# Optimization experiments

Measured on AMD Instinct MI355X. Metric: run time of the kernel, lower is better.

## Reference

```python
import jax, jax.numpy as jnp
import numpy as np

D_MODEL = 1024
N_HEADS = 16
HEAD_DIM = D_MODEL // N_HEADS
WINDOW = 256
N_GLOBAL = 2
EPS = 1e-5


def _layernorm(x, g, b):
    mu = jnp.mean(x, axis=-1, keepdims=True)
    var = jnp.var(x, axis=-1, keepdims=True)
    return (x - mu) * jax.lax.rsqrt(var + EPS) * g + b


def _longformer_mask(T):
    i = jnp.arange(T)[:, None]
    j = jnp.arange(T)[None, :]
    half = WINDOW // 2
    local = (j >= i - half) & (j <= i + half)
    glob = jnp.zeros((T, T), dtype=bool)
    if N_GLOBAL >= 1:
        glob = glob | (i == 0) | (j == 0)
    if N_GLOBAL >= 2 and T > 1:
        glob = glob | (i == T - 1) | (j == T - 1)
    allowed = (local | glob) & (j <= i)  # causal
    neg_inf = jnp.float32(-jnp.inf)
    return jnp.where(allowed, jnp.float32(0.0), neg_inf)[None, None]  # (1,1,T,T)


def setup_inputs() -> dict:
    key = jax.random.key(0)
    ks = jax.random.split(key, 8)
    B, T, D = 2, 2048, D_MODEL
    s = 0.02
    return {
        "x": jax.random.normal(ks[0], (B, T, D), dtype=jnp.float32),
        "ln1_g": jnp.ones((D,), jnp.float32),
        "ln1_b": jnp.zeros((D,), jnp.float32),
        "ln2_g": jnp.ones((D,), jnp.float32),
        "ln2_b": jnp.zeros((D,), jnp.float32),
        "Wq": jax.random.normal(ks[1], (D, D), jnp.float32) * s,
        "Wk": jax.random.normal(ks[2], (D, D), jnp.float32) * s,
        "Wv": jax.random.normal(ks[3], (D, D), jnp.float32) * s,
        "Wo": jax.random.normal(ks[4], (D, D), jnp.float32) * s,
        "bo": jnp.zeros((D,), jnp.float32),
        "W1": jax.random.normal(ks[5], (D, 4 * D), jnp.float32) * s,
        "b1": jnp.zeros((4 * D,), jnp.float32),
        "W2": jax.random.normal(ks[6], (4 * D, D), jnp.float32) * s,
        "b2": jnp.zeros((D,), jnp.float32),
    }


def reference(x, ln1_g, ln1_b, ln2_g, ln2_b, Wq, Wk, Wv, Wo, bo, W1, b1, W2, b2):
    B, T, D = x.shape
    h = _layernorm(x, ln1_g, ln1_b)
    # (B,T,D) -> (B,H,T,hd)
    q = (h @ Wq).reshape(B, T, N_HEADS, HEAD_DIM).transpose(0, 2, 1, 3)
    k = (h @ Wk).reshape(B, T, N_HEADS, HEAD_DIM).transpose(0, 2, 1, 3)
    v = (h @ Wv).reshape(B, T, N_HEADS, HEAD_DIM).transpose(0, 2, 1, 3)
    mask = _longformer_mask(T)
    scores = jnp.einsum("bhqd,bhkd->bhqk", q, k) / np.sqrt(HEAD_DIM) + mask
    attn = jax.nn.softmax(scores, axis=-1)
    out = jnp.einsum("bhqk,bhkd->bhqd", attn, v)
    out = out.transpose(0, 2, 1, 3).reshape(B, T, D)
    x = x + out @ Wo + bo
    h2 = _layernorm(x, ln2_g, ln2_b)
    ffn = jax.nn.gelu(h2 @ W1 + b1, approximate=False) @ W2 + b2
    return x + ffn
```

## Files before the change

kernel.cpp:

```cpp
#include <hip/hip_runtime.h>
#include <cmath>

#define Tseq 2048
#define Dm   1024
#define NHd  16
#define HDim 64
#define Mrows 4096
#define QS   3072
#define PAD  72
#define NSPLIT 16

typedef _Float16 f16;
typedef _Float16 half8 __attribute__((ext_vector_type(8)));
typedef _Float16 half4 __attribute__((ext_vector_type(4)));
typedef float    floatx4 __attribute__((ext_vector_type(4)));

#define ASYNC_COPY16(g, l)                                                       \
  __builtin_amdgcn_global_load_lds((const __attribute__((address_space(1))) void*)(g), \
                                   (__attribute__((address_space(3))) void*)(l), 16, 0, 0)

__device__ __forceinline__ float gelu_f(float v) {
  const float u = 0.7978845608028654f * (v + 0.044715f * v * v * v);
  const float e = __expf(2.0f * u);
  return 0.5f * v * (2.0f - 2.0f / (e + 1.0f));
}

__global__ __launch_bounds__(256) void transp_f16(const float* __restrict__ W,
                                                  f16* __restrict__ Wt, int K, int N) {
  __shared__ float tile[32][33];
  const int n0 = blockIdx.x * 32, k0 = blockIdx.y * 32;
  const int tx = threadIdx.x & 31, ty = threadIdx.x >> 5;
#pragma unroll
  for (int i = 0; i < 32; i += 8)
    tile[ty + i][tx] = W[(size_t)(k0 + ty + i) * N + n0 + tx];
  __syncthreads();
#pragma unroll
  for (int i = 0; i < 32; i += 8)
    Wt[(size_t)(n0 + ty + i) * K + k0 + tx] = (f16)tile[tx][ty + i];
}

__global__ __launch_bounds__(256) void transp_qkv(const float* __restrict__ Wq,
                                                  const float* __restrict__ Wk,
                                                  const float* __restrict__ Wv,
                                                  f16* __restrict__ Wt) {
  __shared__ float tile[32][33];
  const float* W = (blockIdx.z == 0) ? Wq : (blockIdx.z == 1) ? Wk : Wv;
  f16* dst = Wt + (size_t)blockIdx.z * Dm * Dm;
  const int n0 = blockIdx.x * 32, k0 = blockIdx.y * 32;
  const int tx = threadIdx.x & 31, ty = threadIdx.x >> 5;
#pragma unroll
  for (int i = 0; i < 32; i += 8)
    tile[ty + i][tx] = W[(size_t)(k0 + ty + i) * Dm + n0 + tx];
  __syncthreads();
#pragma unroll
  for (int i = 0; i < 32; i += 8)
    dst[(size_t)(n0 + ty + i) * Dm + k0 + tx] = (f16)tile[tx][ty + i];
}

__global__ __launch_bounds__(256) void ln_f16(const float* __restrict__ x,
                                              const float* __restrict__ g,
                                              const float* __restrict__ bb,
                                              f16* __restrict__ out) {
  const int row = blockIdx.x, t = threadIdx.x;
  const float4 v = ((const float4*)(x + (size_t)row * Dm))[t];
  float s  = v.x + v.y + v.z + v.w;
  float ss = v.x * v.x + v.y * v.y + v.z * v.z + v.w * v.w;
#pragma unroll
  for (int m = 32; m >= 1; m >>= 1) { s += __shfl_xor(s, m); ss += __shfl_xor(ss, m); }
  __shared__ float red[8];
  if ((t & 63) == 0) { red[t >> 6] = s; red[4 + (t >> 6)] = ss; }
  __syncthreads();
  const float S  = red[0] + red[1] + red[2] + red[3];
  const float SS = red[4] + red[5] + red[6] + red[7];
  const float mean = S * (1.0f / Dm);
  const float inv  = rsqrtf(SS * (1.0f / Dm) - mean * mean + 1e-5f);
  const float4 gg = ((const float4*)g)[t];
  const float4 bv = ((const float4*)bb)[t];
  half4 o;
  o.x = (f16)(((v.x - mean) * inv) * gg.x + bv.x);
  o.y = (f16)(((v.y - mean) * inv) * gg.y + bv.y);
  o.z = (f16)(((v.z - mean) * inv) * gg.z + bv.z);
  o.w = (f16)(((v.w - mean) * inv) * gg.w + bv.w);
  *((half4*)(out + (size_t)row * Dm) + t) = o;
}

template <int NS>
__global__ __launch_bounds__(256) void reduce_ln(const f16* __restrict__ P,
                                                 const float* __restrict__ resid,
                                                 const float* __restrict__ bias,
                                                 const float* __restrict__ g,
                                                 const float* __restrict__ bb,
                                                 float* __restrict__ x1,
                                                 f16* __restrict__ h) {
  const int row = blockIdx.x, t = threadIdx.x;
  const size_t idx = (size_t)row * (Dm / 4) + t;
  const float4 r = ((const float4*)resid)[idx];
  const float4 b = ((const float4*)bias)[t];
  float4 o; o.x = r.x + b.x; o.y = r.y + b.y; o.z = r.z + b.z; o.w = r.w + b.w;
#pragma unroll
  for (int z = 0; z < NS; ++z) {
    const half4 p = ((const half4*)(P + (size_t)z * Mrows * Dm))[idx];
    o.x += (float)p[0]; o.y += (float)p[1]; o.z += (float)p[2]; o.w += (float)p[3];
  }
  ((float4*)x1)[idx] = o;
  float s  = o.x + o.y + o.z + o.w;
  float ss = o.x * o.x + o.y * o.y + o.z * o.z + o.w * o.w;
#pragma unroll
  for (int m = 32; m >= 1; m >>= 1) { s += __shfl_xor(s, m); ss += __shfl_xor(ss, m); }
  __shared__ float red[8];
  if ((t & 63) == 0) { red[t >> 6] = s; red[4 + (t >> 6)] = ss; }
  __syncthreads();
  const float S  = red[0] + red[1] + red[2] + red[3];
  const float SS = red[4] + red[5] + red[6] + red[7];
  const float mean = S * (1.0f / Dm);
  const float inv  = rsqrtf(SS * (1.0f / Dm) - mean * mean + 1e-5f);
  const float4 gg = ((const float4*)g)[t];
  const float4 bv = ((const float4*)bb)[t];
  half4 oh;
  oh[0] = (f16)(((o.x - mean) * inv) * gg.x + bv.x);
  oh[1] = (f16)(((o.y - mean) * inv) * gg.y + bv.y);
  oh[2] = (f16)(((o.z - mean) * inv) * gg.z + bv.z);
  oh[3] = (f16)(((o.w - mean) * inv) * gg.w + bv.w);
  ((half4*)h)[idx] = oh;
}

template <int NS>
__global__ __launch_bounds__(256) void reduceK(const f16* __restrict__ P,
                                               const float* __restrict__ resid,
                                               const float* __restrict__ bias,
                                               float* __restrict__ out) {
  const int t = blockIdx.x * 256 + threadIdx.x;
  const int col4 = t & (Dm / 4 - 1);
  const float4 r = ((const float4*)resid)[t];
  const float4 b = ((const float4*)bias)[col4];
  float4 o; o.x = r.x + b.x; o.y = r.y + b.y; o.z = r.z + b.z; o.w = r.w + b.w;
#pragma unroll
  for (int z = 0; z < NS; ++z) {
    const half4 p = ((const half4*)(P + (size_t)z * Mrows * Dm))[t];
    o.x += (float)p[0]; o.y += (float)p[1]; o.z += (float)p[2]; o.w += (float)p[3];
  }
  ((float4*)out)[t] = o;
}

template <int EPI>
__global__ __launch_bounds__(256, 4) void gemm_f16(const f16* __restrict__ A,
                                                   const f16* __restrict__ Bt,
                                                   int M, int N, int K, int kLen,
                                                   const float* __restrict__ bias,
                                                   f16* __restrict__ Ch) {
  __shared__ f16 As[128 * 64];
  __shared__ f16 Bs[128 * 64];
  const int tid = threadIdx.x;
  const int m0 = blockIdx.y * 128, n0 = blockIdx.x * 128;
  const int kOff = blockIdx.z * kLen;
  const int w = tid >> 6, l = tid & 63;
  const int wr = (w >> 1) * 64, wc = (w & 1) * 64;
  const int c = l & 15, qq = l >> 4;
  const int cx = c & 7;
  const int srow = tid >> 3;
  const int scol = ((tid & 7) ^ (srow & 7)) * 8;

  floatx4 acc[4][4] = {};

  const f16* Ab = A + (size_t)(m0 + srow) * K + kOff + scol;
  const f16* Bb = Bt + (size_t)(n0 + srow) * K + kOff + scol;

  for (int k0 = 0; k0 < kLen; k0 += 64) {
    __syncthreads();
#pragma unroll
    for (int i = 0; i < 4; ++i) {
      ASYNC_COPY16(Ab + k0 + (size_t)(i * 32) * K, As + i * 2048 + w * 512);
      ASYNC_COPY16(Bb + k0 + (size_t)(i * 32) * K, Bs + i * 2048 + w * 512);
    }
    __syncthreads();
    half8 af[4][2], bfr[4][2];
#pragma unroll
    for (int t = 0; t < 4; ++t) {
      const int ra = (wr + t * 16 + c) * 64;
      af[t][0] = *(const half8*)&As[ra + ((qq ^ cx) * 8)];
      af[t][1] = *(const half8*)&As[ra + (((4 + qq) ^ cx) * 8)];
      const int rb = (wc + t * 16 + c) * 64;
      bfr[t][0] = *(const half8*)&Bs[rb + ((qq ^ cx) * 8)];
      bfr[t][1] = *(const half8*)&Bs[rb + (((4 + qq) ^ cx) * 8)];
    }
#pragma unroll
    for (int ti = 0; ti < 4; ++ti)
#pragma unroll
      for (int tj = 0; tj < 4; ++tj) {
        acc[ti][tj] = __builtin_amdgcn_mfma_f32_16x16x32_f16(af[ti][0], bfr[tj][0], acc[ti][tj], 0, 0, 0);
        acc[ti][tj] = __builtin_amdgcn_mfma_f32_16x16x32_f16(af[ti][1], bfr[tj][1], acc[ti][tj], 0, 0, 0);
      }
  }

  f16* Cw = (EPI == 5) ? (Ch + (size_t)blockIdx.z * M * N) : Ch;
#pragma unroll
  for (int ti = 0; ti < 4; ++ti)
#pragma unroll
    for (int tj = 0; tj < 4; ++tj)
#pragma unroll
      for (int r = 0; r < 4; ++r) {
        const int row = m0 + wr + ti * 16 + qq * 4 + r;
        const int col = n0 + wc + tj * 16 + c;
        const size_t idx = (size_t)row * N + col;
        float v = acc[ti][tj][r];
        if (EPI == 2) {
          Cw[idx] = (f16)gelu_f(v + bias[col]);
        } else {
          Cw[idx] = (f16)v;
        }
      }
}

__global__ __launch_bounds__(256, 4) void attn_win(const f16* __restrict__ qkv,
                                                   f16* __restrict__ ao) {
  __shared__ f16 qs[64 * PAD];
  __shared__ f16 ks[64 * PAD];
  __shared__ f16 vts[64 * PAD];
  __shared__ f16 ps[64 * PAD];
  const int qt = blockIdx.x;
  const int b = blockIdx.y >> 4, hh = blockIdx.y & 15;
  const int q0 = qt * 64;
  const int tid = threadIdx.x, w = tid >> 6, l = tid & 63;
  const int c = l & 15, qq = l >> 4;
  const int wr = w * 16;
  const size_t base = ((size_t)b * Tseq) * QS + hh * HDim;
  const int rr = tid >> 2, ss = (tid & 3) * 16;

  {
    const f16* src = qkv + base + (size_t)(q0 + rr) * QS + ss;
    *(uint4*)&qs[rr * PAD + ss]     = *(const uint4*)src;
    *(uint4*)&qs[rr * PAD + ss + 8] = *(const uint4*)(src + 8);
  }

  float m_run[4], l_run[4];
  floatx4 oacc[4];
#pragma unroll
  for (int r = 0; r < 4; ++r) { m_run[r] = -INFINITY; l_run[r] = 0.f; }
#pragma unroll
  for (int td = 0; td < 4; ++td) oacc[td] = (floatx4){0.f, 0.f, 0.f, 0.f};

  int chunks[4]; int nch = 0;
  if (qt > 2) chunks[nch++] = 0;
  for (int ch = (qt - 2 > 0 ? qt - 2 : 0); ch <= qt; ++ch) chunks[nch++] = ch;

  for (int ci = 0; ci < nch; ++ci) {
    const int j0 = chunks[ci] * 64;
    __syncthreads();
    {
      const f16* srck = qkv + base + 1024 + (size_t)(j0 + rr) * QS + ss;
      *(uint4*)&ks[rr * PAD + ss]     = *(const uint4*)srck;
      *(uint4*)&ks[rr * PAD + ss + 8] = *(const uint4*)(srck + 8);
      const f16* srcv = qkv + base + 2048 + (size_t)(j0 + rr) * QS + ss;
      uint4 va0 = *(const uint4*)srcv;
      uint4 va1 = *(const uint4*)(srcv + 8);
      const f16* e0 = (const f16*)&va0;
      const f16* e1 = (const f16*)&va1;
#pragma unroll
      for (int i = 0; i < 8; ++i) vts[(ss + i) * PAD + rr] = e0[i];
#pragma unroll
      for (int i = 0; i < 8; ++i) vts[(ss + 8 + i) * PAD + rr] = e1[i];
    }
    __syncthreads();

    const half8 a0 = *(const half8*)&qs[(wr + c) * PAD + qq * 8];
    const half8 a1 = *(const half8*)&qs[(wr + c) * PAD + 32 + qq * 8];
    floatx4 sacc[4];
#pragma unroll
    for (int tj = 0; tj < 4; ++tj) {
      const half8 b0 = *(const half8*)&ks[(tj * 16 + c) * PAD + qq * 8];
      const half8 b1 = *(const half8*)&ks[(tj * 16 + c) * PAD + 32 + qq * 8];
      floatx4 s4 = {0.f, 0.f, 0.f, 0.f};
      s4 = __builtin_amdgcn_mfma_f32_16x16x32_f16(a0, b0, s4, 0, 0, 0);
      s4 = __builtin_amdgcn_mfma_f32_16x16x32_f16(a1, b1, s4, 0, 0, 0);
      sacc[tj] = s4;
    }

#pragma unroll
    for (int r = 0; r < 4; ++r) {
      const int ii = q0 + wr + qq * 4 + r;
      float sv[4];
      float mx = -INFINITY;
#pragma unroll
      for (int tj = 0; tj < 4; ++tj) {
        const int jj = j0 + tj * 16 + c;
        const bool allowed = (jj <= ii) && ((ii - jj) <= 128 || jj == 0);
        sv[tj] = allowed ? sacc[tj][r] * 0.125f : -INFINITY;
        mx = fmaxf(mx, sv[tj]);
      }
#pragma unroll
      for (int mm = 8; mm >= 1; mm >>= 1) mx = fmaxf(mx, __shfl_xor(mx, mm));
      const float mn = fmaxf(m_run[r], mx);
      const float alpha = (mn == -INFINITY) ? 1.f : __expf(m_run[r] - mn);
      float sum = 0.f;
      float p[4];
#pragma unroll
      for (int tj = 0; tj < 4; ++tj) { p[tj] = __expf(sv[tj] - mn); sum += p[tj]; }
#pragma unroll
      for (int mm = 8; mm >= 1; mm >>= 1) sum += __shfl_xor(sum, mm);
      l_run[r] = l_run[r] * alpha + sum;
      m_run[r] = mn;
#pragma unroll
      for (int td = 0; td < 4; ++td) oacc[td][r] *= alpha;
#pragma unroll
      for (int tj = 0; tj < 4; ++tj)
        ps[(wr + qq * 4 + r) * PAD + tj * 16 + c] = (f16)p[tj];
    }

    const half8 p0 = *(const half8*)&ps[(wr + c) * PAD + qq * 8];
    const half8 p1 = *(const half8*)&ps[(wr + c) * PAD + 32 + qq * 8];
#pragma unroll
    for (int td = 0; td < 4; ++td) {
      const half8 b0 = *(const half8*)&vts[(td * 16 + c) * PAD + qq * 8];
      const half8 b1 = *(const half8*)&vts[(td * 16 + c) * PAD + 32 + qq * 8];
      oacc[td] = __builtin_amdgcn_mfma_f32_16x16x32_f16(p0, b0, oacc[td], 0, 0, 0);
      oacc[td] = __builtin_amdgcn_mfma_f32_16x16x32_f16(p1, b1, oacc[td], 0, 0, 0);
    }
  }

#pragma unroll
  for (int td = 0; td < 4; ++td)
#pragma unroll
    for (int r = 0; r < 4; ++r) {
      const int ii = q0 + wr + qq * 4 + r;
      ao[((size_t)(b * Tseq + ii)) * Dm + hh * HDim + td * 16 + c] =
          (f16)(oacc[td][r] / l_run[r]);
    }
}

__global__ __launch_bounds__(256) void attn_row_part(const f16* __restrict__ qkv,
                                                     float* __restrict__ part) {
  const int bh = blockIdx.x, sp = blockIdx.y;
  const int b = bh >> 4, hh = bh & 15;
  const int tid = threadIdx.x;
  const size_t base = ((size_t)b * Tseq) * QS + hh * HDim;
  const int j0 = sp * (Tseq / NSPLIT);
  __shared__ float qsh[64];
  __shared__ float ps[128];
  __shared__ float red[4];
  __shared__ float red2[4];
  __shared__ float oacc[4][64];
  if (tid < 64) qsh[tid] = (float)qkv[base + (size_t)(Tseq - 1) * QS + tid] * 0.125f;
  __syncthreads();
  float sv = -INFINITY;
  if (tid < 128) {
    const f16* kr = qkv + base + 1024 + (size_t)(j0 + tid) * QS;
    float a0 = 0.f;
#pragma unroll
    for (int d8 = 0; d8 < 8; ++d8) {
      const half8 kv = *(const half8*)(kr + d8 * 8);
#pragma unroll
      for (int e = 0; e < 8; ++e) a0 = fmaf((float)kv[e], qsh[d8 * 8 + e], a0);
    }
    sv = a0;
  }
  float mx = sv;
#pragma unroll
  for (int mm = 32; mm >= 1; mm >>= 1) mx = fmaxf(mx, __shfl_xor(mx, mm));
  if ((tid & 63) == 0) red[tid >> 6] = mx;
  __syncthreads();
  const float M = fmaxf(red[0], red[1]);
  float p = 0.f;
  if (tid < 128) { p = __expf(sv - M); ps[tid] = p; }
  float sum = p;
#pragma unroll
  for (int mm = 32; mm >= 1; mm >>= 1) sum += __shfl_xor(sum, mm);
  if ((tid & 63) == 0) red2[tid >> 6] = sum;
  __syncthreads();
  const float L = red2[0] + red2[1];
  const int d = tid & 63, pt = tid >> 6;
  const f16* vb = qkv + base + 2048 + d;
  float acc = 0.f;
  for (int j = pt * 32; j < pt * 32 + 32; ++j)
    acc = fmaf(ps[j], (float)vb[(size_t)(j0 + j) * QS], acc);
  oacc[pt][d] = acc;
  __syncthreads();
  if (tid < 64) {
    const float o = oacc[0][tid] + oacc[1][tid] + oacc[2][tid] + oacc[3][tid];
    float* dst = part + ((size_t)bh * NSPLIT + sp) * 66;
    dst[tid] = o;
    if (tid == 0) { dst[64] = M; dst[65] = L; }
  }
}

__global__ __launch_bounds__(64) void attn_row_comb(const float* __restrict__ part,
                                                    f16* __restrict__ ao) {
  const int bh = blockIdx.x;
  const int b = bh >> 4, hh = bh & 15;
  const int tid = threadIdx.x;
  const float* pp = part + (size_t)bh * NSPLIT * 66;
  float M = -INFINITY;
#pragma unroll
  for (int s = 0; s < NSPLIT; ++s) M = fmaxf(M, pp[s * 66 + 64]);
  float L = 0.f, o = 0.f;
#pragma unroll
  for (int s = 0; s < NSPLIT; ++s) {
    const float wgt = __expf(pp[s * 66 + 64] - M);
    L += pp[s * 66 + 65] * wgt;
    o += pp[s * 66 + tid] * wgt;
  }
  ao[((size_t)(b * Tseq + Tseq - 1)) * Dm + hh * HDim + tid] = (f16)(o / L);
}

extern "C" void kernel_launch(void* const* d_in, const int* in_sizes, int n_in,
                              void* d_out, int out_size, void* d_ws, size_t ws_size,
                              hipStream_t stream) {
  (void)in_sizes; (void)n_in; (void)out_size; (void)ws_size;
  const float* x    = (const float*)d_in[0];
  const float* ln1g = (const float*)d_in[1];
  const float* ln1b = (const float*)d_in[2];
  const float* ln2g = (const float*)d_in[3];
  const float* ln2b = (const float*)d_in[4];
  const float* Wq   = (const float*)d_in[5];
  const float* Wk   = (const float*)d_in[6];
  const float* Wv   = (const float*)d_in[7];
  const float* Wo   = (const float*)d_in[8];
  const float* bo   = (const float*)d_in[9];
  const float* W1   = (const float*)d_in[10];
  const float* b1   = (const float*)d_in[11];
  const float* W2   = (const float*)d_in[12];
  const float* b2   = (const float*)d_in[13];
  float* out = (float*)d_out;

  char* w0 = (char*)d_ws;
  size_t off = 0;
  auto take = [&](size_t bytes) -> char* {
    char* p = w0 + off;
    off += (bytes + 255) & ~(size_t)255;
    return p;
  };
  f16*   WqkvT = (f16*)take((size_t)3 * Dm * Dm * 2);
  f16*   WoT   = (f16*)take((size_t)Dm * Dm * 2);
  f16*   W1T   = (f16*)take((size_t)Dm * 4 * Dm * 2);
  f16*   W2T   = (f16*)take((size_t)Dm * 4 * Dm * 2);
  f16*   hF    = (f16*)take((size_t)Mrows * Dm * 2);
  f16*   qkvh  = (f16*)take((size_t)Mrows * QS * 2);
  f16*   attnF = (f16*)take((size_t)Mrows * Dm * 2);
  float* x1    = (float*)take((size_t)Mrows * Dm * 4);
  f16*   h2F   = (f16*)take((size_t)Mrows * Dm * 2);
  f16*   pbuf  = (f16*)take((size_t)4 * Mrows * Dm * 2);
  float* rowp  = (float*)take((size_t)32 * NSPLIT * 66 * 4);
  f16*   ffn1F = qkvh;

  const dim3 blk(256);
  transp_qkv<<<dim3(Dm / 32, Dm / 32, 3), blk, 0, stream>>>(Wq, Wk, Wv, WqkvT);
  transp_f16<<<dim3(Dm / 32, Dm / 32), blk, 0, stream>>>(Wo, WoT, Dm, Dm);
  transp_f16<<<dim3(4 * Dm / 32, Dm / 32), blk, 0, stream>>>(W1, W1T, Dm, 4 * Dm);
  transp_f16<<<dim3(Dm / 32, 4 * Dm / 32), blk, 0, stream>>>(W2, W2T, 4 * Dm, Dm);

  ln_f16<<<Mrows, blk, 0, stream>>>(x, ln1g, ln1b, hF);

  gemm_f16<3><<<dim3(QS / 128, Mrows / 128), blk, 0, stream>>>(hF, WqkvT, Mrows, QS, Dm, Dm, nullptr, qkvh);

  attn_row_part<<<dim3(2 * NHd, NSPLIT), blk, 0, stream>>>(qkvh, rowp);
  attn_win<<<dim3(Tseq / 64, 2 * NHd), blk, 0, stream>>>(qkvh, attnF);
  attn_row_comb<<<dim3(2 * NHd), dim3(64), 0, stream>>>(rowp, attnF);

  gemm_f16<5><<<dim3(Dm / 128, Mrows / 128, 2), blk, 0, stream>>>(attnF, WoT, Mrows, Dm, Dm, Dm / 2, nullptr, pbuf);
  reduce_ln<2><<<Mrows, blk, 0, stream>>>(pbuf, x, bo, ln2g, ln2b, x1, h2F);

  gemm_f16<2><<<dim3(4 * Dm / 128, Mrows / 128), blk, 0, stream>>>(h2F, W1T, Mrows, 4 * Dm, Dm, Dm, b1, ffn1F);

  gemm_f16<5><<<dim3(Dm / 128, Mrows / 128, 4), blk, 0, stream>>>(ffn1F, W2T, Mrows, Dm, 4 * Dm, Dm, nullptr, pbuf);
  reduceK<4><<<Mrows * Dm / 1024, blk, 0, stream>>>(pbuf, x1, b2, out);
}
```

Measured before the change: 348.1 us.

## Fuse split-K reduction into W2 GEMM via atomic tickets; remap split-K grid linearly

The final split-K W2 GEMM now counts finished K-slices per output tile with an atomic ticket, and the last block to arrive sums the fp16 partials, adds the residual and bias, and writes the fp32 output. This removes the separate reduceK launch. Both split-K GEMMs also use a 1D grid with the split index innermost, so the K-slices of one tile are scheduled close together, which may improve L2 reuse of the partials. The cost is threadfences, an atomic per tile, a memset of the counters, and a serialized reduction tail inside one block per tile.

```diff
diff --git a/kernel.cpp b/kernel.cpp
--- a/kernel.cpp
+++ b/kernel.cpp
@@ -124,35 +124,30 @@
   ((half4*)h)[idx] = oh;
 }
 
-template <int NS>
-__global__ __launch_bounds__(256) void reduceK(const f16* __restrict__ P,
-                                               const float* __restrict__ resid,
-                                               const float* __restrict__ bias,
-                                               float* __restrict__ out) {
-  const int t = blockIdx.x * 256 + threadIdx.x;
-  const int col4 = t & (Dm / 4 - 1);
-  const float4 r = ((const float4*)resid)[t];
-  const float4 b = ((const float4*)bias)[col4];
-  float4 o; o.x = r.x + b.x; o.y = r.y + b.y; o.z = r.z + b.z; o.w = r.w + b.w;
-#pragma unroll
-  for (int z = 0; z < NS; ++z) {
-    const half4 p = ((const half4*)(P + (size_t)z * Mrows * Dm))[t];
-    o.x += (float)p[0]; o.y += (float)p[1]; o.z += (float)p[2]; o.w += (float)p[3];
-  }
-  ((float4*)out)[t] = o;
-}
-
-template <int EPI>
+template <int EPI, int LNZ>
 __global__ __launch_bounds__(256, 4) void gemm_f16(const f16* __restrict__ A,
                                                    const f16* __restrict__ Bt,
                                                    int M, int N, int K, int kLen,
                                                    const float* __restrict__ bias,
-                                                   f16* __restrict__ Ch) {
+                                                   f16* __restrict__ Ch,
+                                                   const float* __restrict__ resid,
+                                                   float* __restrict__ Cf,
+                                                   int* __restrict__ cnt) {
+  constexpr int NZ = 1 << LNZ;
   __shared__ f16 As[128 * 64];
   __shared__ f16 Bs[128 * 64];
   const int tid = threadIdx.x;
-  const int m0 = blockIdx.y * 128, n0 = blockIdx.x * 128;
-  const int kOff = blockIdx.z * kLen;
+  int bx, by, bz;
+  if (EPI >= 5) {
+    const int lin = blockIdx.x;
+    bz = lin & (NZ - 1);
+    bx = (lin >> LNZ) & 7;
+    by = lin >> (LNZ + 3);
+  } else {
+    bx = blockIdx.x; by = blockIdx.y; bz = blockIdx.z;
+  }
+  const int m0 = by * 128, n0 = bx * 128;
+  const int kOff = bz * kLen;
   const int w = tid >> 6, l = tid & 63;
   const int wr = (w >> 1) * 64, wc = (w & 1) * 64;
   const int c = l & 15, qq = l >> 4;
@@ -192,7 +187,7 @@
       }
   }
 
-  f16* Cw = (EPI == 5) ? (Ch + (size_t)blockIdx.z * M * N) : Ch;
+  f16* Cw = (EPI >= 5) ? (Ch + (size_t)bz * M * N) : Ch;
 #pragma unroll
   for (int ti = 0; ti < 4; ++ti)
 #pragma unroll
@@ -209,6 +204,31 @@
           Cw[idx] = (f16)v;
         }
       }
+
+  if (EPI == 6) {
+    __shared__ int ticket;
+    __threadfence();
+    __syncthreads();
+    if (tid == 0) ticket = atomicAdd(&cnt[by * 8 + bx], 1);
+    __syncthreads();
+    if (ticket == NZ - 1) {
+      __threadfence();
+      const int ncol4 = N >> 2;
+      for (int e = tid; e < 128 * 32; e += 256) {
+        const int rr2 = e >> 5, c4 = e & 31;
+        const size_t i4 = (size_t)(m0 + rr2) * ncol4 + (n0 >> 2) + c4;
+        const float4 rv = ((const float4*)resid)[i4];
+        const float4 bv = ((const float4*)bias)[(n0 >> 2) + c4];
+        float4 o; o.x = rv.x + bv.x; o.y = rv.y + bv.y; o.z = rv.z + bv.z; o.w = rv.w + bv.w;
+#pragma unroll
+        for (int z = 0; z < NZ; ++z) {
+          const half4 p = ((const half4*)(Ch + (size_t)z * M * N))[i4];
+          o.x += (float)p[0]; o.y += (float)p[1]; o.z += (float)p[2]; o.w += (float)p[3];
+        }
+        ((float4*)Cf)[i4] = o;
+      }
+    }
+  }
 }
 
 __global__ __launch_bounds__(256, 4) void attn_win(const f16* __restrict__ qkv,
@@ -439,9 +459,11 @@
   f16*   h2F   = (f16*)take((size_t)Mrows * Dm * 2);
   f16*   pbuf  = (f16*)take((size_t)4 * Mrows * Dm * 2);
   float* rowp  = (float*)take((size_t)32 * NSPLIT * 66 * 4);
+  int*   cnt   = (int*)take((size_t)256 * 4);
   f16*   ffn1F = qkvh;
 
   const dim3 blk(256);
+  hipMemsetAsync(cnt, 0, 256 * 4, stream);
   transp_qkv<<<dim3(Dm / 32, Dm / 32, 3), blk, 0, stream>>>(Wq, Wk, Wv, WqkvT);
   transp_f16<<<dim3(Dm / 32, Dm / 32), blk, 0, stream>>>(Wo, WoT, Dm, Dm);
   transp_f16<<<dim3(4 * Dm / 32, Dm / 32), blk, 0, stream>>>(W1, W1T, Dm, 4 * Dm);
@@ -449,17 +471,20 @@
 
   ln_f16<<<Mrows, blk, 0, stream>>>(x, ln1g, ln1b, hF);
 
-  gemm_f16<3><<<dim3(QS / 128, Mrows / 128), blk, 0, stream>>>(hF, WqkvT, Mrows, QS, Dm, Dm, nullptr, qkvh);
+  gemm_f16<3, 0><<<dim3(QS / 128, Mrows / 128), blk, 0, stream>>>(
+      hF, WqkvT, Mrows, QS, Dm, Dm, nullptr, qkvh, nullptr, nullptr, nullptr);
 
   attn_row_part<<<dim3(2 * NHd, NSPLIT), blk, 0, stream>>>(qkvh, rowp);
   attn_win<<<dim3(Tseq / 64, 2 * NHd), blk, 0, stream>>>(qkvh, attnF);
   attn_row_comb<<<dim3(2 * NHd), dim3(64), 0, stream>>>(rowp, attnF);
 
-  gemm_f16<5><<<dim3(Dm / 128, Mrows / 128, 2), blk, 0, stream>>>(attnF, WoT, Mrows, Dm, Dm, Dm / 2, nullptr, pbuf);
+  gemm_f16<5, 1><<<dim3(512), blk, 0, stream>>>(
+      attnF, WoT, Mrows, Dm, Dm, Dm / 2, nullptr, pbuf, nullptr, nullptr, nullptr);
   reduce_ln<2><<<Mrows, blk, 0, stream>>>(pbuf, x, bo, ln2g, ln2b, x1, h2F);
 
-  gemm_f16<2><<<dim3(4 * Dm / 128, Mrows / 128), blk, 0, stream>>>(h2F, W1T, Mrows, 4 * Dm, Dm, Dm, b1, ffn1F);
-
-  gemm_f16<5><<<dim3(Dm / 128, Mrows / 128, 4), blk, 0, stream>>>(ffn1F, W2T, Mrows, Dm, 4 * Dm, Dm, nullptr, pbuf);
-  reduceK<4><<<Mrows * Dm / 1024, blk, 0, stream>>>(pbuf, x1, b2, out);
-}
+  gemm_f16<2, 0><<<dim3(4 * Dm / 128, Mrows / 128), blk, 0, stream>>>(
+      h2F, W1T, Mrows, 4 * Dm, Dm, Dm, b1, ffn1F, nullptr, nullptr, nullptr);
+
+  gemm_f16<6, 2><<<dim3(1024), blk, 0, stream>>>(
+      ffn1F, W2T, Mrows, Dm, 4 * Dm, Dm, b2, pbuf, x1, out, cnt);
+}
```

Measured after the change: 613.7 us. 76.3% more time.
